# Kernel tuning notes

Hardware: AMD Instinct MI355X
Metric: run time of the kernel (lower is better)

Reference implementation:

```python
import jax, jax.numpy as jnp
import numpy as np

N_NODES = 50000
N_EDGES = 640000
D = 128        # node_dim
T = 128        # time_dim
EDGE_IN = 2 * D + 1 + T   # 385
NODE_IN = 2 * D + T       # 384


def setup_inputs() -> dict:
    key = jax.random.key(0)
    ks = jax.random.split(key, 16)
    inp = {
        "h": jax.random.normal(ks[0], (N_NODES, D), jnp.float32),
        "diff_cart": jax.random.normal(ks[1], (N_EDGES, 3), jnp.float32),
        "dist_sq": jax.random.uniform(ks[2], (N_EDGES, 1), jnp.float32),
        "edge_src": jax.random.randint(ks[3], (N_EDGES,), 0, N_NODES),
        "edge_dst": jax.random.randint(ks[4], (N_EDGES,), 0, N_NODES),
        "t_emb_edges": jax.random.normal(ks[5], (N_EDGES, T), jnp.float32),
        "t_emb_nodes": jax.random.normal(ks[6], (N_NODES, T), jnp.float32),
        # edge_mlp: Linear(385,128) SiLU Linear(128,128) SiLU  (weights stored [in,out])
        "We1": jax.random.normal(ks[7], (EDGE_IN, D), jnp.float32) / np.sqrt(EDGE_IN),
        "be1": jnp.zeros((D,), jnp.float32),
        "We2": jax.random.normal(ks[8], (D, D), jnp.float32) / np.sqrt(D),
        "be2": jnp.zeros((D,), jnp.float32),
        # coord_mlp: Linear(128,128) SiLU Linear(128,1, bias=False)
        "Wc1": jax.random.normal(ks[9], (D, D), jnp.float32) / np.sqrt(D),
        "bc1": jnp.zeros((D,), jnp.float32),
        "Wc2": jax.random.normal(ks[10], (D, 1), jnp.float32) / np.sqrt(D),
        # node_mlp: Linear(384,128) SiLU Linear(128,128)
        "Wn1": jax.random.normal(ks[11], (NODE_IN, D), jnp.float32) / np.sqrt(NODE_IN),
        "bn1": jnp.zeros((D,), jnp.float32),
        "Wn2": jax.random.normal(ks[12], (D, D), jnp.float32) / np.sqrt(D),
        "bn2": jnp.zeros((D,), jnp.float32),
    }
    return inp


def reference(h, diff_cart, dist_sq, edge_src, edge_dst, t_emb_edges, t_emb_nodes,
              We1, be1, We2, be2, Wc1, bc1, Wc2, Wn1, bn1, Wn2, bn2):
    silu = jax.nn.silu
    n = h.shape[0]
    # gather + edge MLP
    edge_input = jnp.concatenate([h[edge_src], h[edge_dst], dist_sq, t_emb_edges], axis=-1)  # [E, 385]
    m_ij = silu(silu(edge_input @ We1 + be1) @ We2 + be2)  # [E, D]
    # coord MLP -> scalar weight per edge
    coord_weights = silu(m_ij @ Wc1 + bc1) @ Wc2  # [E, 1]
    coord_shift = diff_cart * coord_weights  # [E, 3]
    # scatter-add back to nodes
    coord_update = jax.ops.segment_sum(coord_shift, edge_src, num_segments=n)  # [N, 3]
    m_i = jax.ops.segment_sum(m_ij, edge_dst, num_segments=n)  # [N, D]
    # node MLP + residual
    node_input = jnp.concatenate([h, m_i, t_emb_nodes], axis=-1)  # [N, 384]
    h_update = h + silu(node_input @ Wn1 + bn1) @ Wn2 + bn2
    # note: torch Linear applies bias after matmul; rewrite faithfully:
    h_update = h + (silu(node_input @ Wn1 + bn1) @ Wn2 + bn2)
    return (h_update, coord_update)
```

## Files before the change

kernel.cpp:

```cpp
#include <hip/hip_runtime.h>
#include <hip/hip_bf16.h>

#define N_NODES 50000
#define N_EDGES 640000
#define D 128
#define T 128
#define KE 384
#define KN 384
#define MT 64

typedef __attribute__((ext_vector_type(8))) short  bf16x8;
typedef __attribute__((ext_vector_type(4))) float  f32x4;
typedef __attribute__((ext_vector_type(4))) unsigned short u16x4;
typedef __attribute__((ext_vector_type(8))) unsigned short u16x8;

__device__ __forceinline__ float silu_f(float x) { return x / (1.0f + __expf(-x)); }

__device__ __forceinline__ unsigned short f2bf(float x) {
    union { float f; unsigned u; } v; v.f = x;
    unsigned r = v.u + 0x7fffu + ((v.u >> 16) & 1u);
    return (unsigned short)(r >> 16);
}

__device__ __forceinline__ float bf2f(unsigned short u) {
    union { unsigned u; float f; } v; v.u = ((unsigned)u) << 16;
    return v.f;
}

__global__ __launch_bounds__(256) void prep_weights(
    const float* __restrict__ We1, const float* __restrict__ We2,
    const float* __restrict__ Wc1, const float* __restrict__ Wn1,
    const float* __restrict__ Wn2,
    unsigned short* __restrict__ Wt1, unsigned short* __restrict__ Wt2,
    unsigned short* __restrict__ Wtc1, unsigned short* __restrict__ Wtn1,
    unsigned short* __restrict__ Wtn2, float* __restrict__ w1dist)
{
    const int c = blockIdx.x;
    const int t = threadIdx.x;
    for (int k = t; k < KE; k += 256) {
        float v = (k < 256) ? We1[(size_t)k * D + c] : We1[(size_t)(k + 1) * D + c];
        Wt1[(size_t)c * KE + k] = f2bf(v);
    }
    if (t == 0) w1dist[c] = We1[(size_t)256 * D + c];
    for (int k = t; k < D; k += 256) {
        Wt2 [(size_t)c * D + k] = f2bf(We2[(size_t)k * D + c]);
        Wtc1[(size_t)c * D + k] = f2bf(Wc1[(size_t)k * D + c]);
        Wtn2[(size_t)c * D + k] = f2bf(Wn2[(size_t)k * D + c]);
    }
    for (int k = t; k < KN; k += 256) {
        Wtn1[(size_t)c * KN + k] = f2bf(Wn1[(size_t)k * D + c]);
    }
}

__global__ __launch_bounds__(256) void hist_kernel(const int* __restrict__ edst, int* __restrict__ cnt) {
    const int i = blockIdx.x * 256 + threadIdx.x;
    if (i < N_EDGES) atomicAdd(&cnt[edst[i]], 1);
}

__global__ __launch_bounds__(1024) void scan_kernel(const int* __restrict__ cnt,
                                                    int* __restrict__ off, int* __restrict__ cur) {
    __shared__ int part[1024];
    const int t = threadIdx.x;
    const int PER = 49;
    const int base = t * PER;
    int s = 0;
    for (int i = 0; i < PER; ++i) { int idx = base + i; if (idx < N_NODES) s += cnt[idx]; }
    part[t] = s; __syncthreads();
    for (int d = 1; d < 1024; d <<= 1) {
        int v = (t >= d) ? part[t - d] : 0;
        __syncthreads();
        part[t] += v;
        __syncthreads();
    }
    int excl = (t == 0) ? 0 : part[t - 1];
    for (int i = 0; i < PER; ++i) {
        int idx = base + i;
        if (idx < N_NODES) { off[idx] = excl; cur[idx] = excl; excl += cnt[idx]; }
    }
    if (t == 1023) off[N_NODES] = excl;
}

__global__ __launch_bounds__(256) void fill_kernel(const int* __restrict__ edst,
                                                   int* __restrict__ cur, int* __restrict__ eidx) {
    const int i = blockIdx.x * 256 + threadIdx.x;
    if (i < N_EDGES) {
        const int pos = atomicAdd(&cur[edst[i]], 1);
        eidx[pos] = i;
    }
}

__global__ __launch_bounds__(256) void edge_kernel(
    const float* __restrict__ h, const float* __restrict__ diff_cart,
    const float* __restrict__ dist_sq, const int* __restrict__ esrc,
    const int* __restrict__ edst, const float* __restrict__ temb,
    const unsigned short* __restrict__ Wt1, const float* __restrict__ be1,
    const unsigned short* __restrict__ Wt2, const float* __restrict__ be2,
    const unsigned short* __restrict__ Wtc1, const float* __restrict__ bc1,
    const float* __restrict__ wc2, const float* __restrict__ w1dist,
    unsigned short* __restrict__ mij, float* __restrict__ coord_out)
{
    __shared__ __align__(16) unsigned short smem[MT * KE];
    __shared__ float cwp[4 * MT];
    __shared__ int s_src[MT];
    __shared__ float s_dist[MT];

    char* sbytes = (char*)smem;
    const int tid = threadIdx.x, blk = blockIdx.x;
    const int w = tid >> 6, l = tid & 63, lo = l & 15, hi = l >> 4;
    const int cb = w * 32;

    if (tid < MT) {
        s_src[tid]  = esrc[blk * MT + tid];
        s_dist[tid] = dist_sq[blk * MT + tid];
    }

    {
        const int r = tid >> 2, q = tid & 3;
        const int ge = blk * MT + r;
        const int src = esrc[ge], dst = edst[ge];
        const float* hs = h + (size_t)src * D;
        const float* hd = h + (size_t)dst * D;
        const float* tp = temb + (size_t)ge * T;
        #pragma unroll
        for (int i = 0; i < 12; ++i) {
            const int col = (q * 12 + i) * 8;
            const float* p = (col < 128) ? (hs + col) : (col < 256) ? (hd + col - 128) : (tp + col - 256);
            f32x4 v0 = *(const f32x4*)p;
            f32x4 v1 = *(const f32x4*)(p + 4);
            u16x8 u;
            #pragma unroll
            for (int j = 0; j < 4; ++j) { u[j] = f2bf(v0[j]); u[4 + j] = f2bf(v1[j]); }
            int b = (r * (KE * 2) + col * 2) ^ ((r & 7) << 4);
            *(u16x8*)(sbytes + b) = u;
        }
    }
    __syncthreads();

    f32x4 acc[2][4];
    #pragma unroll
    for (int ci = 0; ci < 2; ++ci)
        #pragma unroll
        for (int ej = 0; ej < 4; ++ej) acc[ci][ej] = (f32x4){0.f, 0.f, 0.f, 0.f};
    {
        const unsigned short* w0 = Wt1 + (size_t)(cb + lo) * KE + hi * 8;
        const unsigned short* w1 = Wt1 + (size_t)(cb + 16 + lo) * KE + hi * 8;
        #pragma unroll
        for (int kk = 0; kk < 12; ++kk) {
            bf16x8 a0 = *(const bf16x8*)(w0 + kk * 32);
            bf16x8 a1 = *(const bf16x8*)(w1 + kk * 32);
            bf16x8 bfr[4];
            #pragma unroll
            for (int ej = 0; ej < 4; ++ej) {
                int b = ((16 * ej + lo) * (KE * 2) + kk * 64 + hi * 16) ^ ((lo & 7) << 4);
                bfr[ej] = *(const bf16x8*)(sbytes + b);
            }
            #pragma unroll
            for (int ej = 0; ej < 4; ++ej) {
                acc[0][ej] = __builtin_amdgcn_mfma_f32_16x16x32_bf16(a0, bfr[ej], acc[0][ej], 0, 0, 0);
                acc[1][ej] = __builtin_amdgcn_mfma_f32_16x16x32_bf16(a1, bfr[ej], acc[1][ej], 0, 0, 0);
            }
        }
    }
    float bv[2][4], wd[2][4];
    #pragma unroll
    for (int ci = 0; ci < 2; ++ci) {
        f32x4 b4 = *(const f32x4*)(be1 + cb + 16 * ci + hi * 4);
        f32x4 w4 = *(const f32x4*)(w1dist + cb + 16 * ci + hi * 4);
        #pragma unroll
        for (int r = 0; r < 4; ++r) { bv[ci][r] = b4[r]; wd[ci][r] = w4[r]; }
    }
    __syncthreads();

    #pragma unroll
    for (int ci = 0; ci < 2; ++ci)
        #pragma unroll
        for (int ej = 0; ej < 4; ++ej) {
            const float dv = s_dist[16 * ej + lo];
            u16x4 u;
            #pragma unroll
            for (int r = 0; r < 4; ++r) u[r] = f2bf(silu_f(acc[ci][ej][r] + bv[ci][r] + dv * wd[ci][r]));
            const int e = 16 * ej + lo, c0 = cb + 16 * ci + hi * 4;
            int b = (e * 256 + c0 * 2) ^ ((e & 7) << 4);
            *(u16x4*)(sbytes + b) = u;
        }
    __syncthreads();

    #pragma unroll
    for (int ci = 0; ci < 2; ++ci)
        #pragma unroll
        for (int ej = 0; ej < 4; ++ej) acc[ci][ej] = (f32x4){0.f, 0.f, 0.f, 0.f};
    {
        const unsigned short* w0 = Wt2 + (size_t)(cb + lo) * D + hi * 8;
        const unsigned short* w1 = Wt2 + (size_t)(cb + 16 + lo) * D + hi * 8;
        #pragma unroll
        for (int kk = 0; kk < 4; ++kk) {
            bf16x8 a0 = *(const bf16x8*)(w0 + kk * 32);
            bf16x8 a1 = *(const bf16x8*)(w1 + kk * 32);
            bf16x8 bfr[4];
            #pragma unroll
            for (int ej = 0; ej < 4; ++ej) {
                int b = ((16 * ej + lo) * 256 + kk * 64 + hi * 16) ^ ((lo & 7) << 4);
                bfr[ej] = *(const bf16x8*)(sbytes + b);
            }
            #pragma unroll
            for (int ej = 0; ej < 4; ++ej) {
                acc[0][ej] = __builtin_amdgcn_mfma_f32_16x16x32_bf16(a0, bfr[ej], acc[0][ej], 0, 0, 0);
                acc[1][ej] = __builtin_amdgcn_mfma_f32_16x16x32_bf16(a1, bfr[ej], acc[1][ej], 0, 0, 0);
            }
        }
    }
    #pragma unroll
    for (int ci = 0; ci < 2; ++ci) {
        f32x4 b4 = *(const f32x4*)(be2 + cb + 16 * ci + hi * 4);
        #pragma unroll
        for (int r = 0; r < 4; ++r) bv[ci][r] = b4[r];
    }

    #pragma unroll
    for (int ci = 0; ci < 2; ++ci)
        #pragma unroll
        for (int ej = 0; ej < 4; ++ej) {
            const int e = 16 * ej + lo, c0 = cb + 16 * ci + hi * 4;
            u16x4 u;
            #pragma unroll
            for (int r = 0; r < 4; ++r) u[r] = f2bf(silu_f(acc[ci][ej][r] + bv[ci][r]));
            int b = 16384 + ((e * 256 + c0 * 2) ^ ((e & 7) << 4));
            *(u16x4*)(sbytes + b) = u;
        }
    __syncthreads();

    {
        const int r = tid >> 2, q = tid & 3;
        unsigned short* gp = mij + (size_t)(blk * MT + r) * D + q * 32;
        #pragma unroll
        for (int i = 0; i < 4; ++i) {
            int b = 16384 + ((r * 256 + q * 64 + i * 16) ^ ((r & 7) << 4));
            *(u16x8*)(gp + i * 8) = *(const u16x8*)(sbytes + b);
        }
    }

    #pragma unroll
    for (int ci = 0; ci < 2; ++ci)
        #pragma unroll
        for (int ej = 0; ej < 4; ++ej) acc[ci][ej] = (f32x4){0.f, 0.f, 0.f, 0.f};
    {
        const unsigned short* w0 = Wtc1 + (size_t)(cb + lo) * D + hi * 8;
        const unsigned short* w1 = Wtc1 + (size_t)(cb + 16 + lo) * D + hi * 8;
        #pragma unroll
        for (int kk = 0; kk < 4; ++kk) {
            bf16x8 a0 = *(const bf16x8*)(w0 + kk * 32);
            bf16x8 a1 = *(const bf16x8*)(w1 + kk * 32);
            bf16x8 bfr[4];
            #pragma unroll
            for (int ej = 0; ej < 4; ++ej) {
                int b = 16384 + (((16 * ej + lo) * 256 + kk * 64 + hi * 16) ^ ((lo & 7) << 4));
                bfr[ej] = *(const bf16x8*)(sbytes + b);
            }
            #pragma unroll
            for (int ej = 0; ej < 4; ++ej) {
                acc[0][ej] = __builtin_amdgcn_mfma_f32_16x16x32_bf16(a0, bfr[ej], acc[0][ej], 0, 0, 0);
                acc[1][ej] = __builtin_amdgcn_mfma_f32_16x16x32_bf16(a1, bfr[ej], acc[1][ej], 0, 0, 0);
            }
        }
    }
    {
        float wcv[2][4], bcv[2][4];
        #pragma unroll
        for (int ci = 0; ci < 2; ++ci) {
            f32x4 w4 = *(const f32x4*)(wc2 + cb + 16 * ci + hi * 4);
            f32x4 b4 = *(const f32x4*)(bc1 + cb + 16 * ci + hi * 4);
            #pragma unroll
            for (int r = 0; r < 4; ++r) { wcv[ci][r] = w4[r]; bcv[ci][r] = b4[r]; }
        }
        float p[4] = {0.f, 0.f, 0.f, 0.f};
        #pragma unroll
        for (int ci = 0; ci < 2; ++ci)
            #pragma unroll
            for (int ej = 0; ej < 4; ++ej)
                #pragma unroll
                for (int r = 0; r < 4; ++r)
                    p[ej] += silu_f(acc[ci][ej][r] + bcv[ci][r]) * wcv[ci][r];
        #pragma unroll
        for (int ej = 0; ej < 4; ++ej) {
            p[ej] += __shfl_xor(p[ej], 16, 64);
            p[ej] += __shfl_xor(p[ej], 32, 64);
        }
        if (hi == 0) {
            #pragma unroll
            for (int ej = 0; ej < 4; ++ej) cwp[w * MT + 16 * ej + lo] = p[ej];
        }
    }
    __syncthreads();
    if (tid < MT) {
        const float cw = cwp[tid] + cwp[MT + tid] + cwp[2 * MT + tid] + cwp[3 * MT + tid];
        const int ge = blk * MT + tid;
        const int s = s_src[tid];
        const float* dc = diff_cart + (size_t)ge * 3;
        unsafeAtomicAdd(coord_out + (size_t)s * 3 + 0, dc[0] * cw);
        unsafeAtomicAdd(coord_out + (size_t)s * 3 + 1, dc[1] * cw);
        unsafeAtomicAdd(coord_out + (size_t)s * 3 + 2, dc[2] * cw);
    }
}

__global__ __launch_bounds__(256) void node_kernel(
    const float* __restrict__ h, const float* __restrict__ tembn,
    const int* __restrict__ off, const int* __restrict__ eidx,
    const unsigned short* __restrict__ mij,
    const unsigned short* __restrict__ Wtn1, const float* __restrict__ bn1,
    const unsigned short* __restrict__ Wtn2, const float* __restrict__ bn2,
    float* __restrict__ out)
{
    __shared__ __align__(16) unsigned short smem[MT * KN];
    char* sbytes = (char*)smem;
    const int tid = threadIdx.x, blk = blockIdx.x;
    const int w = tid >> 6, l = tid & 63, lo = l & 15, hi = l >> 4;
    const int cb = w * 32;

    {
        const int r = tid >> 2, q = tid & 3;
        const int n = blk * MT + r;
        const bool valid = (n < N_NODES);
        {
            const float* hp = h + (size_t)n * D + q * 32;
            #pragma unroll
            for (int g = 0; g < 4; ++g) {
                u16x8 u;
                if (valid) {
                    f32x4 v0 = *(const f32x4*)(hp + g * 8);
                    f32x4 v1 = *(const f32x4*)(hp + g * 8 + 4);
                    #pragma unroll
                    for (int j = 0; j < 4; ++j) { u[j] = f2bf(v0[j]); u[4 + j] = f2bf(v1[j]); }
                } else {
                    #pragma unroll
                    for (int j = 0; j < 8; ++j) u[j] = 0;
                }
                const int col = q * 32 + g * 8;
                int b = (r * (KN * 2) + col * 2) ^ ((r & 7) << 4);
                *(u16x8*)(sbytes + b) = u;
            }
        }
        {
            const float* tp = tembn + (size_t)n * T + q * 32;
            #pragma unroll
            for (int g = 0; g < 4; ++g) {
                u16x8 u;
                if (valid) {
                    f32x4 v0 = *(const f32x4*)(tp + g * 8);
                    f32x4 v1 = *(const f32x4*)(tp + g * 8 + 4);
                    #pragma unroll
                    for (int j = 0; j < 4; ++j) { u[j] = f2bf(v0[j]); u[4 + j] = f2bf(v1[j]); }
                } else {
                    #pragma unroll
                    for (int j = 0; j < 8; ++j) u[j] = 0;
                }
                const int col = 256 + q * 32 + g * 8;
                int b = (r * (KN * 2) + col * 2) ^ ((r & 7) << 4);
                *(u16x8*)(sbytes + b) = u;
            }
        }
        {
            float acc[32];
            #pragma unroll
            for (int j = 0; j < 32; ++j) acc[j] = 0.f;
            const int st = valid ? off[n] : 0;
            const int en = valid ? off[n + 1] : 0;
            for (int j = st; j < en; ++j) {
                const int e = eidx[j];
                const unsigned short* mp = mij + (size_t)e * D + q * 32;
                #pragma unroll
                for (int g = 0; g < 4; ++g) {
                    u16x8 v = *(const u16x8*)(mp + g * 8);
                    #pragma unroll
                    for (int k = 0; k < 8; ++k) acc[g * 8 + k] += bf2f(v[k]);
                }
            }
            #pragma unroll
            for (int g = 0; g < 4; ++g) {
                u16x8 u;
                #pragma unroll
                for (int k = 0; k < 8; ++k) u[k] = f2bf(acc[g * 8 + k]);
                const int col = 128 + q * 32 + g * 8;
                int b = (r * (KN * 2) + col * 2) ^ ((r & 7) << 4);
                *(u16x8*)(sbytes + b) = u;
            }
        }
    }
    __syncthreads();

    f32x4 acc[2][4];
    #pragma unroll
    for (int ci = 0; ci < 2; ++ci)
        #pragma unroll
        for (int ej = 0; ej < 4; ++ej) acc[ci][ej] = (f32x4){0.f, 0.f, 0.f, 0.f};
    {
        const unsigned short* w0 = Wtn1 + (size_t)(cb + lo) * KN + hi * 8;
        const unsigned short* w1 = Wtn1 + (size_t)(cb + 16 + lo) * KN + hi * 8;
        #pragma unroll
        for (int kk = 0; kk < 12; ++kk) {
            bf16x8 a0 = *(const bf16x8*)(w0 + kk * 32);
            bf16x8 a1 = *(const bf16x8*)(w1 + kk * 32);
            bf16x8 bfr[4];
            #pragma unroll
            for (int ej = 0; ej < 4; ++ej) {
                int b = ((16 * ej + lo) * (KN * 2) + kk * 64 + hi * 16) ^ ((lo & 7) << 4);
                bfr[ej] = *(const bf16x8*)(sbytes + b);
            }
            #pragma unroll
            for (int ej = 0; ej < 4; ++ej) {
                acc[0][ej] = __builtin_amdgcn_mfma_f32_16x16x32_bf16(a0, bfr[ej], acc[0][ej], 0, 0, 0);
                acc[1][ej] = __builtin_amdgcn_mfma_f32_16x16x32_bf16(a1, bfr[ej], acc[1][ej], 0, 0, 0);
            }
        }
    }
    float bv[2][4];
    #pragma unroll
    for (int ci = 0; ci < 2; ++ci) {
        f32x4 b4 = *(const f32x4*)(bn1 + cb + 16 * ci + hi * 4);
        #pragma unroll
        for (int r = 0; r < 4; ++r) bv[ci][r] = b4[r];
    }
    __syncthreads();

    #pragma unroll
    for (int ci = 0; ci < 2; ++ci)
        #pragma unroll
        for (int ej = 0; ej < 4; ++ej) {
            u16x4 u;
            #pragma unroll
            for (int r = 0; r < 4; ++r) u[r] = f2bf(silu_f(acc[ci][ej][r] + bv[ci][r]));
            const int e = 16 * ej + lo, c0 = cb + 16 * ci + hi * 4;
            int b = (e * 256 + c0 * 2) ^ ((e & 7) << 4);
            *(u16x4*)(sbytes + b) = u;
        }
    __syncthreads();

    #pragma unroll
    for (int ci = 0; ci < 2; ++ci)
        #pragma unroll
        for (int ej = 0; ej < 4; ++ej) acc[ci][ej] = (f32x4){0.f, 0.f, 0.f, 0.f};
    {
        const unsigned short* w0 = Wtn2 + (size_t)(cb + lo) * D + hi * 8;
        const unsigned short* w1 = Wtn2 + (size_t)(cb + 16 + lo) * D + hi * 8;
        #pragma unroll
        for (int kk = 0; kk < 4; ++kk) {
            bf16x8 a0 = *(const bf16x8*)(w0 + kk * 32);
            bf16x8 a1 = *(const bf16x8*)(w1 + kk * 32);
            bf16x8 bfr[4];
            #pragma unroll
            for (int ej = 0; ej < 4; ++ej) {
                int b = ((16 * ej + lo) * 256 + kk * 64 + hi * 16) ^ ((lo & 7) << 4);
                bfr[ej] = *(const bf16x8*)(sbytes + b);
            }
            #pragma unroll
            for (int ej = 0; ej < 4; ++ej) {
                acc[0][ej] = __builtin_amdgcn_mfma_f32_16x16x32_bf16(a0, bfr[ej], acc[0][ej], 0, 0, 0);
                acc[1][ej] = __builtin_amdgcn_mfma_f32_16x16x32_bf16(a1, bfr[ej], acc[1][ej], 0, 0, 0);
            }
        }
    }
    #pragma unroll
    for (int ci = 0; ci < 2; ++ci) {
        f32x4 b4 = *(const f32x4*)(bn2 + cb + 16 * ci + hi * 4);
        #pragma unroll
        for (int r = 0; r < 4; ++r) bv[ci][r] = b4[r];
    }

    #pragma unroll
    for (int ej = 0; ej < 4; ++ej) {
        const int e = 16 * ej + lo;
        const int n2 = blk * MT + e;
        if (n2 < N_NODES) {
            #pragma unroll
            for (int ci = 0; ci < 2; ++ci) {
                const int c0 = cb + 16 * ci + hi * 4;
                f32x4 hres = *(const f32x4*)(h + (size_t)n2 * D + c0);
                f32x4 o;
                #pragma unroll
                for (int r = 0; r < 4; ++r) o[r] = acc[ci][ej][r] + bv[ci][r] + hres[r];
                *(f32x4*)(out + (size_t)n2 * D + c0) = o;
            }
        }
    }
}

extern "C" void kernel_launch(void* const* d_in, const int* in_sizes, int n_in,
                              void* d_out, int out_size, void* d_ws, size_t ws_size,
                              hipStream_t stream) {
    const float* h    = (const float*)d_in[0];
    const float* diff = (const float*)d_in[1];
    const float* dsq  = (const float*)d_in[2];
    const int*   esrc = (const int*)d_in[3];
    const int*   edst = (const int*)d_in[4];
    const float* tEe  = (const float*)d_in[5];
    const float* tEn  = (const float*)d_in[6];
    const float* We1  = (const float*)d_in[7];
    const float* be1  = (const float*)d_in[8];
    const float* We2  = (const float*)d_in[9];
    const float* be2  = (const float*)d_in[10];
    const float* Wc1  = (const float*)d_in[11];
    const float* bc1  = (const float*)d_in[12];
    const float* Wc2  = (const float*)d_in[13];
    const float* Wn1  = (const float*)d_in[14];
    const float* bn1  = (const float*)d_in[15];
    const float* Wn2  = (const float*)d_in[16];
    const float* bn2  = (const float*)d_in[17];

    float* out = (float*)d_out;
    float* coord_out = out + (size_t)N_NODES * D;

    char* ws = (char*)d_ws;
    size_t off_b = 0;
    unsigned short* mij = (unsigned short*)(ws + off_b); off_b += (size_t)N_EDGES * D * 2;
    unsigned short* Wt1  = (unsigned short*)(ws + off_b); off_b += (size_t)D * KE * 2;
    unsigned short* Wt2  = (unsigned short*)(ws + off_b); off_b += (size_t)D * D * 2;
    unsigned short* Wtc1 = (unsigned short*)(ws + off_b); off_b += (size_t)D * D * 2;
    unsigned short* Wtn1 = (unsigned short*)(ws + off_b); off_b += (size_t)D * KN * 2;
    unsigned short* Wtn2 = (unsigned short*)(ws + off_b); off_b += (size_t)D * D * 2;
    float* w1dist = (float*)(ws + off_b); off_b += (size_t)D * 4;
    int* cnt  = (int*)(ws + off_b); off_b += (size_t)N_NODES * 4;
    int* csoff= (int*)(ws + off_b); off_b += (size_t)(N_NODES + 1) * 4;
    int* cur  = (int*)(ws + off_b); off_b += (size_t)N_NODES * 4;
    int* eidx = (int*)(ws + off_b); off_b += (size_t)N_EDGES * 4;

    hipMemsetAsync(cnt, 0, (size_t)N_NODES * 4, stream);
    hipMemsetAsync(coord_out, 0, (size_t)N_NODES * 3 * sizeof(float), stream);

    prep_weights<<<dim3(D), dim3(256), 0, stream>>>(We1, We2, Wc1, Wn1, Wn2,
                                                    Wt1, Wt2, Wtc1, Wtn1, Wtn2, w1dist);
    hist_kernel<<<dim3((N_EDGES + 255) / 256), dim3(256), 0, stream>>>(edst, cnt);
    scan_kernel<<<dim3(1), dim3(1024), 0, stream>>>(cnt, csoff, cur);
    fill_kernel<<<dim3((N_EDGES + 255) / 256), dim3(256), 0, stream>>>(edst, cur, eidx);
    edge_kernel<<<dim3(N_EDGES / MT), dim3(256), 0, stream>>>(
        h, diff, dsq, esrc, edst, tEe, Wt1, be1, Wt2, be2, Wtc1, bc1, Wc2, w1dist, mij, coord_out);
    node_kernel<<<dim3((N_NODES + MT - 1) / MT), dim3(256), 0, stream>>>(
        h, tEn, csoff, eidx, mij, Wtn1, bn1, Wtn2, bn2, out);
}
```

Before: 1.153 ms.

## Fuse m_ij segment-sum into edge kernel via dst-sorted edges and run-length atomics

The edge kernel now walks edges in dst-sorted order (through eidx). It sums consecutive same-destination rows of m_ij in shared memory and issues fp32 atomics into an m_i buffer, so the bf16 m_ij round-trip through global memory and the CSR gather in the node kernel are gone. The node kernel then loads m_i directly, like h and t_emb. Further changes: packed bf16 conversion instructions, hoisting the second and third layer weights into registers, s_setprio around the MFMA blocks, and occupancy hints in launch_bounds. The costs are scattered access to h, temb and diff_cart, since edges are no longer read in order, plus atomics and an extra memset of m_i.

```diff
diff --git a/kernel.cpp b/kernel.cpp
--- a/kernel.cpp
+++ b/kernel.cpp
@@ -11,8 +11,8 @@
 
 typedef __attribute__((ext_vector_type(8))) short  bf16x8;
 typedef __attribute__((ext_vector_type(4))) float  f32x4;
-typedef __attribute__((ext_vector_type(4))) unsigned short u16x4;
-typedef __attribute__((ext_vector_type(8))) unsigned short u16x8;
+typedef __attribute__((ext_vector_type(2))) unsigned u32x2;
+typedef __attribute__((ext_vector_type(4))) unsigned u32x4;
 
 __device__ __forceinline__ float silu_f(float x) { return x / (1.0f + __expf(-x)); }
 
@@ -25,6 +25,12 @@
 __device__ __forceinline__ float bf2f(unsigned short u) {
     union { unsigned u; float f; } v; v.u = ((unsigned)u) << 16;
     return v.f;
+}
+
+__device__ __forceinline__ unsigned cvtpk(float a, float b) {
+    unsigned r;
+    asm("v_cvt_pk_bf16_f32 %0, %1, %2" : "=v"(r) : "v"(a), "v"(b));
+    return r;
 }
 
 __global__ __launch_bounds__(256) void prep_weights(
@@ -89,19 +95,20 @@
     }
 }
 
-__global__ __launch_bounds__(256) void edge_kernel(
+__global__ __launch_bounds__(256, 3) void edge_kernel(
     const float* __restrict__ h, const float* __restrict__ diff_cart,
     const float* __restrict__ dist_sq, const int* __restrict__ esrc,
     const int* __restrict__ edst, const float* __restrict__ temb,
+    const int* __restrict__ eidx,
     const unsigned short* __restrict__ Wt1, const float* __restrict__ be1,
     const unsigned short* __restrict__ Wt2, const float* __restrict__ be2,
     const unsigned short* __restrict__ Wtc1, const float* __restrict__ bc1,
     const float* __restrict__ wc2, const float* __restrict__ w1dist,
-    unsigned short* __restrict__ mij, float* __restrict__ coord_out)
+    float* __restrict__ m_i, float* __restrict__ coord_out)
 {
     __shared__ __align__(16) unsigned short smem[MT * KE];
     __shared__ float cwp[4 * MT];
-    __shared__ int s_src[MT];
+    __shared__ int s_ge[MT], s_src[MT], s_dst[MT];
     __shared__ float s_dist[MT];
 
     char* sbytes = (char*)smem;
@@ -110,16 +117,19 @@
     const int cb = w * 32;
 
     if (tid < MT) {
-        s_src[tid]  = esrc[blk * MT + tid];
-        s_dist[tid] = dist_sq[blk * MT + tid];
-    }
+        const int ge = eidx[blk * MT + tid];
+        s_ge[tid]   = ge;
+        s_src[tid]  = esrc[ge];
+        s_dst[tid]  = edst[ge];
+        s_dist[tid] = dist_sq[ge];
+    }
+    __syncthreads();
 
     {
         const int r = tid >> 2, q = tid & 3;
-        const int ge = blk * MT + r;
-        const int src = esrc[ge], dst = edst[ge];
-        const float* hs = h + (size_t)src * D;
-        const float* hd = h + (size_t)dst * D;
+        const int ge = s_ge[r];
+        const float* hs = h + (size_t)s_src[r] * D;
+        const float* hd = h + (size_t)s_dst[r] * D;
         const float* tp = temb + (size_t)ge * T;
         #pragma unroll
         for (int i = 0; i < 12; ++i) {
@@ -127,11 +137,11 @@
             const float* p = (col < 128) ? (hs + col) : (col < 256) ? (hd + col - 128) : (tp + col - 256);
             f32x4 v0 = *(const f32x4*)p;
             f32x4 v1 = *(const f32x4*)(p + 4);
-            u16x8 u;
-            #pragma unroll
-            for (int j = 0; j < 4; ++j) { u[j] = f2bf(v0[j]); u[4 + j] = f2bf(v1[j]); }
+            u32x4 u;
+            u[0] = cvtpk(v0[0], v0[1]); u[1] = cvtpk(v0[2], v0[3]);
+            u[2] = cvtpk(v1[0], v1[1]); u[3] = cvtpk(v1[2], v1[3]);
             int b = (r * (KE * 2) + col * 2) ^ ((r & 7) << 4);
-            *(u16x8*)(sbytes + b) = u;
+            *(u32x4*)(sbytes + b) = u;
         }
     }
     __syncthreads();
@@ -154,12 +164,21 @@
                 int b = ((16 * ej + lo) * (KE * 2) + kk * 64 + hi * 16) ^ ((lo & 7) << 4);
                 bfr[ej] = *(const bf16x8*)(sbytes + b);
             }
+            __builtin_amdgcn_s_setprio(1);
             #pragma unroll
             for (int ej = 0; ej < 4; ++ej) {
                 acc[0][ej] = __builtin_amdgcn_mfma_f32_16x16x32_bf16(a0, bfr[ej], acc[0][ej], 0, 0, 0);
                 acc[1][ej] = __builtin_amdgcn_mfma_f32_16x16x32_bf16(a1, bfr[ej], acc[1][ej], 0, 0, 0);
             }
-        }
+            __builtin_amdgcn_s_setprio(0);
+        }
+    }
+    bf16x8 w2a[4], w2b[4];
+    {
+        const unsigned short* p0 = Wt2 + (size_t)(cb + lo) * D + hi * 8;
+        const unsigned short* p1 = Wt2 + (size_t)(cb + 16 + lo) * D + hi * 8;
+        #pragma unroll
+        for (int kk = 0; kk < 4; ++kk) { w2a[kk] = *(const bf16x8*)(p0 + kk * 32); w2b[kk] = *(const bf16x8*)(p1 + kk * 32); }
     }
     float bv[2][4], wd[2][4];
     #pragma unroll
@@ -176,12 +195,14 @@
         #pragma unroll
         for (int ej = 0; ej < 4; ++ej) {
             const float dv = s_dist[16 * ej + lo];
-            u16x4 u;
-            #pragma unroll
-            for (int r = 0; r < 4; ++r) u[r] = f2bf(silu_f(acc[ci][ej][r] + bv[ci][r] + dv * wd[ci][r]));
+            float s0 = silu_f(acc[ci][ej][0] + bv[ci][0] + dv * wd[ci][0]);
+            float s1 = silu_f(acc[ci][ej][1] + bv[ci][1] + dv * wd[ci][1]);
+            float s2 = silu_f(acc[ci][ej][2] + bv[ci][2] + dv * wd[ci][2]);
+            float s3 = silu_f(acc[ci][ej][3] + bv[ci][3] + dv * wd[ci][3]);
+            u32x2 u; u[0] = cvtpk(s0, s1); u[1] = cvtpk(s2, s3);
             const int e = 16 * ej + lo, c0 = cb + 16 * ci + hi * 4;
             int b = (e * 256 + c0 * 2) ^ ((e & 7) << 4);
-            *(u16x4*)(sbytes + b) = u;
+            *(u32x2*)(sbytes + b) = u;
         }
     __syncthreads();
 
@@ -190,24 +211,29 @@
         #pragma unroll
         for (int ej = 0; ej < 4; ++ej) acc[ci][ej] = (f32x4){0.f, 0.f, 0.f, 0.f};
     {
-        const unsigned short* w0 = Wt2 + (size_t)(cb + lo) * D + hi * 8;
-        const unsigned short* w1 = Wt2 + (size_t)(cb + 16 + lo) * D + hi * 8;
         #pragma unroll
         for (int kk = 0; kk < 4; ++kk) {
-            bf16x8 a0 = *(const bf16x8*)(w0 + kk * 32);
-            bf16x8 a1 = *(const bf16x8*)(w1 + kk * 32);
             bf16x8 bfr[4];
             #pragma unroll
             for (int ej = 0; ej < 4; ++ej) {
                 int b = ((16 * ej + lo) * 256 + kk * 64 + hi * 16) ^ ((lo & 7) << 4);
                 bfr[ej] = *(const bf16x8*)(sbytes + b);
             }
-            #pragma unroll
-            for (int ej = 0; ej < 4; ++ej) {
-                acc[0][ej] = __builtin_amdgcn_mfma_f32_16x16x32_bf16(a0, bfr[ej], acc[0][ej], 0, 0, 0);
-                acc[1][ej] = __builtin_amdgcn_mfma_f32_16x16x32_bf16(a1, bfr[ej], acc[1][ej], 0, 0, 0);
-            }
-        }
+            __builtin_amdgcn_s_setprio(1);
+            #pragma unroll
+            for (int ej = 0; ej < 4; ++ej) {
+                acc[0][ej] = __builtin_amdgcn_mfma_f32_16x16x32_bf16(w2a[kk], bfr[ej], acc[0][ej], 0, 0, 0);
+                acc[1][ej] = __builtin_amdgcn_mfma_f32_16x16x32_bf16(w2b[kk], bfr[ej], acc[1][ej], 0, 0, 0);
+            }
+            __builtin_amdgcn_s_setprio(0);
+        }
+    }
+    bf16x8 w3a[4], w3b[4];
+    {
+        const unsigned short* p0 = Wtc1 + (size_t)(cb + lo) * D + hi * 8;
+        const unsigned short* p1 = Wtc1 + (size_t)(cb + 16 + lo) * D + hi * 8;
+        #pragma unroll
+        for (int kk = 0; kk < 4; ++kk) { w3a[kk] = *(const bf16x8*)(p0 + kk * 32); w3b[kk] = *(const bf16x8*)(p1 + kk * 32); }
     }
     #pragma unroll
     for (int ci = 0; ci < 2; ++ci) {
@@ -221,48 +247,58 @@
         #pragma unroll
         for (int ej = 0; ej < 4; ++ej) {
             const int e = 16 * ej + lo, c0 = cb + 16 * ci + hi * 4;
-            u16x4 u;
-            #pragma unroll
-            for (int r = 0; r < 4; ++r) u[r] = f2bf(silu_f(acc[ci][ej][r] + bv[ci][r]));
+            float s0 = silu_f(acc[ci][ej][0] + bv[ci][0]);
+            float s1 = silu_f(acc[ci][ej][1] + bv[ci][1]);
+            float s2 = silu_f(acc[ci][ej][2] + bv[ci][2]);
+            float s3 = silu_f(acc[ci][ej][3] + bv[ci][3]);
+            u32x2 u; u[0] = cvtpk(s0, s1); u[1] = cvtpk(s2, s3);
             int b = 16384 + ((e * 256 + c0 * 2) ^ ((e & 7) << 4));
-            *(u16x4*)(sbytes + b) = u;
-        }
-    __syncthreads();
-
-    {
-        const int r = tid >> 2, q = tid & 3;
-        unsigned short* gp = mij + (size_t)(blk * MT + r) * D + q * 32;
-        #pragma unroll
-        for (int i = 0; i < 4; ++i) {
-            int b = 16384 + ((r * 256 + q * 64 + i * 16) ^ ((r & 7) << 4));
-            *(u16x8*)(gp + i * 8) = *(const u16x8*)(sbytes + b);
-        }
-    }
+            *(u32x2*)(sbytes + b) = u;
+        }
+    __syncthreads();
 
     #pragma unroll
     for (int ci = 0; ci < 2; ++ci)
         #pragma unroll
         for (int ej = 0; ej < 4; ++ej) acc[ci][ej] = (f32x4){0.f, 0.f, 0.f, 0.f};
     {
-        const unsigned short* w0 = Wtc1 + (size_t)(cb + lo) * D + hi * 8;
-        const unsigned short* w1 = Wtc1 + (size_t)(cb + 16 + lo) * D + hi * 8;
         #pragma unroll
         for (int kk = 0; kk < 4; ++kk) {
-            bf16x8 a0 = *(const bf16x8*)(w0 + kk * 32);
-            bf16x8 a1 = *(const bf16x8*)(w1 + kk * 32);
             bf16x8 bfr[4];
             #pragma unroll
             for (int ej = 0; ej < 4; ++ej) {
                 int b = 16384 + (((16 * ej + lo) * 256 + kk * 64 + hi * 16) ^ ((lo & 7) << 4));
                 bfr[ej] = *(const bf16x8*)(sbytes + b);
             }
-            #pragma unroll
-            for (int ej = 0; ej < 4; ++ej) {
-                acc[0][ej] = __builtin_amdgcn_mfma_f32_16x16x32_bf16(a0, bfr[ej], acc[0][ej], 0, 0, 0);
-                acc[1][ej] = __builtin_amdgcn_mfma_f32_16x16x32_bf16(a1, bfr[ej], acc[1][ej], 0, 0, 0);
-            }
-        }
-    }
+            __builtin_amdgcn_s_setprio(1);
+            #pragma unroll
+            for (int ej = 0; ej < 4; ++ej) {
+                acc[0][ej] = __builtin_amdgcn_mfma_f32_16x16x32_bf16(w3a[kk], bfr[ej], acc[0][ej], 0, 0, 0);
+                acc[1][ej] = __builtin_amdgcn_mfma_f32_16x16x32_bf16(w3b[kk], bfr[ej], acc[1][ej], 0, 0, 0);
+            }
+            __builtin_amdgcn_s_setprio(0);
+        }
+    }
+
+    {
+        const int c = tid & 127;
+        const int rbase = (tid >> 7) * 32;
+        float accr = 0.f;
+        int dprev = s_dst[rbase];
+        #pragma unroll 8
+        for (int i = 0; i < 32; ++i) {
+            const int r = rbase + i;
+            const int d = s_dst[r];
+            if (d != dprev) {
+                unsafeAtomicAdd(m_i + (size_t)dprev * D + c, accr);
+                accr = 0.f; dprev = d;
+            }
+            int b = 16384 + ((r * 256 + c * 2) ^ ((r & 7) << 4));
+            accr += bf2f(*(const unsigned short*)(sbytes + b));
+        }
+        unsafeAtomicAdd(m_i + (size_t)dprev * D + c, accr);
+    }
+
     {
         float wcv[2][4], bcv[2][4];
         #pragma unroll
@@ -293,7 +329,7 @@
     __syncthreads();
     if (tid < MT) {
         const float cw = cwp[tid] + cwp[MT + tid] + cwp[2 * MT + tid] + cwp[3 * MT + tid];
-        const int ge = blk * MT + tid;
+        const int ge = s_ge[tid];
         const int s = s_src[tid];
         const float* dc = diff_cart + (size_t)ge * 3;
         unsafeAtomicAdd(coord_out + (size_t)s * 3 + 0, dc[0] * cw);
@@ -302,10 +338,9 @@
     }
 }
 
-__global__ __launch_bounds__(256) void node_kernel(
-    const float* __restrict__ h, const float* __restrict__ tembn,
-    const int* __restrict__ off, const int* __restrict__ eidx,
-    const unsigned short* __restrict__ mij,
+__global__ __launch_bounds__(256, 3) void node_kernel(
+    const float* __restrict__ h, const float* __restrict__ m_i,
+    const float* __restrict__ tembn,
     const unsigned short* __restrict__ Wtn1, const float* __restrict__ bn1,
     const unsigned short* __restrict__ Wtn2, const float* __restrict__ bn2,
     float* __restrict__ out)
@@ -320,69 +355,24 @@
         const int r = tid >> 2, q = tid & 3;
         const int n = blk * MT + r;
         const bool valid = (n < N_NODES);
-        {
-            const float* hp = h + (size_t)n * D + q * 32;
-            #pragma unroll
-            for (int g = 0; g < 4; ++g) {
-                u16x8 u;
-                if (valid) {
-                    f32x4 v0 = *(const f32x4*)(hp + g * 8);
-                    f32x4 v1 = *(const f32x4*)(hp + g * 8 + 4);
-                    #pragma unroll
-                    for (int j = 0; j < 4; ++j) { u[j] = f2bf(v0[j]); u[4 + j] = f2bf(v1[j]); }
-                } else {
-                    #pragma unroll
-                    for (int j = 0; j < 8; ++j) u[j] = 0;
-                }
-                const int col = q * 32 + g * 8;
-                int b = (r * (KN * 2) + col * 2) ^ ((r & 7) << 4);
-                *(u16x8*)(sbytes + b) = u;
-            }
-        }
-        {
-            const float* tp = tembn + (size_t)n * T + q * 32;
-            #pragma unroll
-            for (int g = 0; g < 4; ++g) {
-                u16x8 u;
-                if (valid) {
-                    f32x4 v0 = *(const f32x4*)(tp + g * 8);
-                    f32x4 v1 = *(const f32x4*)(tp + g * 8 + 4);
-                    #pragma unroll
-                    for (int j = 0; j < 4; ++j) { u[j] = f2bf(v0[j]); u[4 + j] = f2bf(v1[j]); }
-                } else {
-                    #pragma unroll
-                    for (int j = 0; j < 8; ++j) u[j] = 0;
-                }
-                const int col = 256 + q * 32 + g * 8;
-                int b = (r * (KN * 2) + col * 2) ^ ((r & 7) << 4);
-                *(u16x8*)(sbytes + b) = u;
-            }
-        }
-        {
-            float acc[32];
-            #pragma unroll
-            for (int j = 0; j < 32; ++j) acc[j] = 0.f;
-            const int st = valid ? off[n] : 0;
-            const int en = valid ? off[n + 1] : 0;
-            for (int j = st; j < en; ++j) {
-                const int e = eidx[j];
-                const unsigned short* mp = mij + (size_t)e * D + q * 32;
-                #pragma unroll
-                for (int g = 0; g < 4; ++g) {
-                    u16x8 v = *(const u16x8*)(mp + g * 8);
-                    #pragma unroll
-                    for (int k = 0; k < 8; ++k) acc[g * 8 + k] += bf2f(v[k]);
-                }
-            }
-            #pragma unroll
-            for (int g = 0; g < 4; ++g) {
-                u16x8 u;
-                #pragma unroll
-                for (int k = 0; k < 8; ++k) u[k] = f2bf(acc[g * 8 + k]);
-                const int col = 128 + q * 32 + g * 8;
-                int b = (r * (KN * 2) + col * 2) ^ ((r & 7) << 4);
-                *(u16x8*)(sbytes + b) = u;
-            }
+        const float* hp = h + (size_t)n * D;
+        const float* mp = m_i + (size_t)n * D;
+        const float* tp = tembn + (size_t)n * T;
+        #pragma unroll
+        for (int i = 0; i < 12; ++i) {
+            const int col = (q * 12 + i) * 8;
+            u32x4 u;
+            if (valid) {
+                const float* p = (col < 128) ? (hp + col) : (col < 256) ? (mp + col - 128) : (tp + col - 256);
+                f32x4 v0 = *(const f32x4*)p;
+                f32x4 v1 = *(const f32x4*)(p + 4);
+                u[0] = cvtpk(v0[0], v0[1]); u[1] = cvtpk(v0[2], v0[3]);
+                u[2] = cvtpk(v1[0], v1[1]); u[3] = cvtpk(v1[2], v1[3]);
+            } else {
+                u[0] = u[1] = u[2] = u[3] = 0u;
+            }
+            int b = (r * (KN * 2) + col * 2) ^ ((r & 7) << 4);
+            *(u32x4*)(sbytes + b) = u;
         }
     }
     __syncthreads();
@@ -405,12 +395,21 @@
                 int b = ((16 * ej + lo) * (KN * 2) + kk * 64 + hi * 16) ^ ((lo & 7) << 4);
                 bfr[ej] = *(const bf16x8*)(sbytes + b);
             }
+            __builtin_amdgcn_s_setprio(1);
             #pragma unroll
             for (int ej = 0; ej < 4; ++ej) {
                 acc[0][ej] = __builtin_amdgcn_mfma_f32_16x16x32_bf16(a0, bfr[ej], acc[0][ej], 0, 0, 0);
                 acc[1][ej] = __builtin_amdgcn_mfma_f32_16x16x32_bf16(a1, bfr[ej], acc[1][ej], 0, 0, 0);
             }
-        }
+            __builtin_amdgcn_s_setprio(0);
+        }
+    }
+    bf16x8 w2a[4], w2b[4];
+    {
+        const unsigned short* p0 = Wtn2 + (size_t)(cb + lo) * D + hi * 8;
+        const unsigned short* p1 = Wtn2 + (size_t)(cb + 16 + lo) * D + hi * 8;
+        #pragma unroll
+        for (int kk = 0; kk < 4; ++kk) { w2a[kk] = *(const bf16x8*)(p0 + kk * 32); w2b[kk] = *(const bf16x8*)(p1 + kk * 32); }
     }
     float bv[2][4];
     #pragma unroll
@@ -425,12 +424,14 @@
     for (int ci = 0; ci < 2; ++ci)
         #pragma unroll
         for (int ej = 0; ej < 4; ++ej) {
-            u16x4 u;
-            #pragma unroll
-            for (int r = 0; r < 4; ++r) u[r] = f2bf(silu_f(acc[ci][ej][r] + bv[ci][r]));
+            float s0 = silu_f(acc[ci][ej][0] + bv[ci][0]);
+            float s1 = silu_f(acc[ci][ej][1] + bv[ci][1]);
+            float s2 = silu_f(acc[ci][ej][2] + bv[ci][2]);
+            float s3 = silu_f(acc[ci][ej][3] + bv[ci][3]);
+            u32x2 u; u[0] = cvtpk(s0, s1); u[1] = cvtpk(s2, s3);
             const int e = 16 * ej + lo, c0 = cb + 16 * ci + hi * 4;
             int b = (e * 256 + c0 * 2) ^ ((e & 7) << 4);
-            *(u16x4*)(sbytes + b) = u;
+            *(u32x2*)(sbytes + b) = u;
         }
     __syncthreads();
 
@@ -439,23 +440,21 @@
         #pragma unroll
         for (int ej = 0; ej < 4; ++ej) acc[ci][ej] = (f32x4){0.f, 0.f, 0.f, 0.f};
     {
-        const unsigned short* w0 = Wtn2 + (size_t)(cb + lo) * D + hi * 8;
-        const unsigned short* w1 = Wtn2 + (size_t)(cb + 16 + lo) * D + hi * 8;
         #pragma unroll
         for (int kk = 0; kk < 4; ++kk) {
-            bf16x8 a0 = *(const bf16x8*)(w0 + kk * 32);
-            bf16x8 a1 = *(const bf16x8*)(w1 + kk * 32);
             bf16x8 bfr[4];
             #pragma unroll
             for (int ej = 0; ej < 4; ++ej) {
                 int b = ((16 * ej + lo) * 256 + kk * 64 + hi * 16) ^ ((lo & 7) << 4);
                 bfr[ej] = *(const bf16x8*)(sbytes + b);
             }
-            #pragma unroll
-            for (int ej = 0; ej < 4; ++ej) {
-                acc[0][ej] = __builtin_amdgcn_mfma_f32_16x16x32_bf16(a0, bfr[ej], acc[0][ej], 0, 0, 0);
-                acc[1][ej] = __builtin_amdgcn_mfma_f32_16x16x32_bf16(a1, bfr[ej], acc[1][ej], 0, 0, 0);
-            }
+            __builtin_amdgcn_s_setprio(1);
+            #pragma unroll
+            for (int ej = 0; ej < 4; ++ej) {
+                acc[0][ej] = __builtin_amdgcn_mfma_f32_16x16x32_bf16(w2a[kk], bfr[ej], acc[0][ej], 0, 0, 0);
+                acc[1][ej] = __builtin_amdgcn_mfma_f32_16x16x32_bf16(w2b[kk], bfr[ej], acc[1][ej], 0, 0, 0);
+            }
+            __builtin_amdgcn_s_setprio(0);
         }
     }
     #pragma unroll
@@ -510,7 +509,7 @@
 
     char* ws = (char*)d_ws;
     size_t off_b = 0;
-    unsigned short* mij = (unsigned short*)(ws + off_b); off_b += (size_t)N_EDGES * D * 2;
+    float* m_i = (float*)(ws + off_b); off_b += (size_t)N_NODES * D * 4;
     unsigned short* Wt1  = (unsigned short*)(ws + off_b); off_b += (size_t)D * KE * 2;
     unsigned short* Wt2  = (unsigned short*)(ws + off_b); off_b += (size_t)D * D * 2;
     unsigned short* Wtc1 = (unsigned short*)(ws + off_b); off_b += (size_t)D * D * 2;
@@ -523,6 +522,7 @@
     int* eidx = (int*)(ws + off_b); off_b += (size_t)N_EDGES * 4;
 
     hipMemsetAsync(cnt, 0, (size_t)N_NODES * 4, stream);
+    hipMemsetAsync(m_i, 0, (size_t)N_NODES * D * 4, stream);
     hipMemsetAsync(coord_out, 0, (size_t)N_NODES * 3 * sizeof(float), stream);
 
     prep_weights<<<dim3(D), dim3(256), 0, stream>>>(We1, We2, Wc1, Wn1, Wn2,
@@ -531,7 +531,7 @@
     scan_kernel<<<dim3(1), dim3(1024), 0, stream>>>(cnt, csoff, cur);
     fill_kernel<<<dim3((N_EDGES + 255) / 256), dim3(256), 0, stream>>>(edst, cur, eidx);
     edge_kernel<<<dim3(N_EDGES / MT), dim3(256), 0, stream>>>(
-        h, diff, dsq, esrc, edst, tEe, Wt1, be1, Wt2, be2, Wtc1, bc1, Wc2, w1dist, mij, coord_out);
+        h, diff, dsq, esrc, edst, tEe, eidx, Wt1, be1, Wt2, be2, Wtc1, bc1, Wc2, w1dist, m_i, coord_out);
     node_kernel<<<dim3((N_NODES + MT - 1) / MT), dim3(256), 0, stream>>>(
-        h, tEn, csoff, eidx, mij, Wtn1, bn1, Wtn2, bn2, out);
-}
+        h, m_i, tEn, Wtn1, bn1, Wtn2, bn2, out);
+}
```

Result: faster. 1.099 ms (-4.7%).
